# Optimization experiments

Hardware: AMD Instinct MI355X
Metric: run time of the kernel (lower is better)

The kernel has to match this reference:

```python
import jax, jax.numpy as jnp
import numpy as np

EPS = 1e-08


def _phi(x, W):
    # Performer-style positive random features for the softmax kernel.
    # x: [..., d], W: [d, m]
    d = x.shape[-1]
    m = W.shape[-1]
    proj = jnp.einsum('...d,dm->...m', x, W) * (d ** -0.25)
    sq = jnp.sum(x * x, axis=-1, keepdims=True) / (2.0 * jnp.sqrt(jnp.float32(d)))
    return jnp.exp(proj - sq) * (m ** -0.5)


def setup_inputs() -> dict:
    key = jax.random.key(0)
    k1, k2, k3 = jax.random.split(key, 3)
    B, L, D = 8, 2048, 512
    K = 4
    m = 256
    content_amp = jax.random.normal(k1, (B, L, D), dtype=jnp.float32)
    style_amp = jax.random.normal(k2, (B, K, L, D), dtype=jnp.float32)
    W = jax.random.normal(k3, (D, m), dtype=jnp.float32)
    return {"content_amp": content_amp, "style_amp": style_amp, "W": W}


def reference(content_amp, style_amp, W):
    B, K, L, D = style_amp.shape
    style_seq = style_amp.reshape(B, K * L, D)          # [B, KL, D]
    phi_q = _phi(content_amp, W)                         # [B, Lq, m]
    phi_k = _phi(style_seq, W)                           # [B, KL, m]
    S = jnp.einsum('bkm,bkd->bmd', phi_k, style_seq)     # [B, m, D]
    Z = jnp.sum(phi_k, axis=1)                           # [B, m]
    num = jnp.einsum('blm,bmd->bld', phi_q, S)           # [B, Lq, D]
    den = jnp.einsum('blm,bm->bl', phi_q, Z)[..., None] + EPS
    f_a = num / den
    amp_updated = content_amp + f_a
    return (amp_updated, f_a)
```

## Files before the change

### kernel.cpp

```cpp
#include <hip/hip_runtime.h>
#include <hip/hip_bf16.h>
#include <math.h>

typedef short  s16x8 __attribute__((ext_vector_type(8)));
typedef short  s16x4 __attribute__((ext_vector_type(4)));
typedef float  f32x4 __attribute__((ext_vector_type(4)));

#define DD 512
#define MM 256
#define BB 8
#define LL 2048
#define KLT 8192

#define S1f     0.21022410381342864f
#define INV2SDf 0.02209708691207961f
#define S2f     0.0625f
#define EPSV    1e-8f

__device__ __forceinline__ ushort f2b(float f) {
    __hip_bfloat16 h = __float2bfloat16(f);
    return *reinterpret_cast<ushort*>(&h);
}
__device__ __forceinline__ float b2f(ushort u) {
    union { unsigned u32; float f; } x; x.u32 = ((unsigned)u) << 16; return x.f;
}

__global__ __launch_bounds__(256) void convert_rows(const float* __restrict__ X,
                                                    ushort* __restrict__ Xb,
                                                    float* __restrict__ Sq) {
    const int row  = blockIdx.x * 4 + (threadIdx.x >> 6);
    const int lane = threadIdx.x & 63;
    const float4* src = (const float4*)(X + (size_t)row * DD);
    float4 v0 = src[lane];
    float4 v1 = src[lane + 64];
    float s = v0.x * v0.x + v0.y * v0.y + v0.z * v0.z + v0.w * v0.w
            + v1.x * v1.x + v1.y * v1.y + v1.z * v1.z + v1.w * v1.w;
    s16x4* dst = (s16x4*)(Xb + (size_t)row * DD);
    s16x4 o0, o1;
    o0[0] = (short)f2b(v0.x); o0[1] = (short)f2b(v0.y);
    o0[2] = (short)f2b(v0.z); o0[3] = (short)f2b(v0.w);
    o1[0] = (short)f2b(v1.x); o1[1] = (short)f2b(v1.y);
    o1[2] = (short)f2b(v1.z); o1[3] = (short)f2b(v1.w);
    dst[lane]      = o0;
    dst[lane + 64] = o1;
#pragma unroll
    for (int off = 32; off; off >>= 1) s += __shfl_down(s, off);
    if (lane == 0) Sq[row] = s * INV2SDf;
}

__global__ __launch_bounds__(256) void prep_w(const float* __restrict__ W,
                                              ushort* __restrict__ Wt) {
    __shared__ ushort lds[64 * 78];
    const int t = threadIdx.x;
    const int dt = blockIdx.x;
    const int mt = blockIdx.y;
    {
        int r = t >> 2, c0 = (t & 3) * 16;
        const float4* src = (const float4*)(W + (size_t)(dt * 64 + r) * MM + mt * 64 + c0);
#pragma unroll
        for (int i = 0; i < 4; ++i) {
            float4 v = src[i];
            lds[r * 78 + c0 + 4 * i + 0] = f2b(v.x);
            lds[r * 78 + c0 + 4 * i + 1] = f2b(v.y);
            lds[r * 78 + c0 + 4 * i + 2] = f2b(v.z);
            lds[r * 78 + c0 + 4 * i + 3] = f2b(v.w);
        }
    }
    __syncthreads();
    {
        int m = t >> 2, d0 = (t & 3) * 16;
        ushort* dst = Wt + (size_t)(mt * 64 + m) * DD + dt * 64 + d0;
#pragma unroll
        for (int j = 0; j < 16; ++j) dst[j] = lds[(d0 + j) * 78 + m];
    }
}

__global__ __launch_bounds__(256) void transpose_k(const ushort* __restrict__ Sb,
                                                   ushort* __restrict__ StyT) {
    __shared__ ushort lds[64 * 72];
    const int t = threadIdx.x;
    const int klt = blockIdx.x;
    const int dt  = blockIdx.y;
    const int b   = blockIdx.z;
    {
        int r = t >> 2, c0 = (t & 3) * 16;
        const ushort* src = Sb + ((size_t)b * KLT + klt * 64 + r) * DD + dt * 64 + c0;
        *(s16x8*)(lds + r * 72 + c0)     = *(const s16x8*)(src);
        *(s16x8*)(lds + r * 72 + c0 + 8) = *(const s16x8*)(src + 8);
    }
    __syncthreads();
    {
        int d = t >> 2, k0 = (t & 3) * 16;
        s16x8 o0, o1;
#pragma unroll
        for (int j = 0; j < 8; ++j) o0[j] = (short)lds[(k0 + j) * 72 + d];
#pragma unroll
        for (int j = 0; j < 8; ++j) o1[j] = (short)lds[(k0 + 8 + j) * 72 + d];
        ushort* dst = StyT + ((size_t)b * DD + dt * 64 + d) * KLT + klt * 64 + k0;
        *(s16x8*)(dst)     = o0;
        *(s16x8*)(dst + 8) = o1;
    }
}

__device__ __forceinline__ void gemm128(const ushort* __restrict__ A, int lda,
                                        const ushort* __restrict__ B, int ldb,
                                        int rowbase, int colbase, int k0, int k1,
                                        ushort* sA, ushort* sB, f32x4 acc[4][4]) {
    const int t = threadIdx.x;
    const int l = t & 63, w = t >> 6;
    const int wr = (w >> 1) * 64, wc = (w & 1) * 64;
    const int fr = l & 15, fg = l >> 4;
    const int srow = t >> 1, shalf = t & 1;

    for (int kk = k0; kk < k1; kk += 32) {
        {
            const ushort* src = A + (size_t)(rowbase + srow) * lda + kk + shalf * 16;
            *(s16x8*)(sA + srow * 40 + shalf * 16)     = *(const s16x8*)(src);
            *(s16x8*)(sA + srow * 40 + shalf * 16 + 8) = *(const s16x8*)(src + 8);
        }
        {
            const ushort* src = B + (size_t)(colbase + srow) * ldb + kk + shalf * 16;
            *(s16x8*)(sB + srow * 40 + shalf * 16)     = *(const s16x8*)(src);
            *(s16x8*)(sB + srow * 40 + shalf * 16 + 8) = *(const s16x8*)(src + 8);
        }
        __syncthreads();
        s16x8 a[4], b[4];
#pragma unroll
        for (int mi = 0; mi < 4; ++mi)
            a[mi] = *(const s16x8*)(sA + (wr + mi * 16 + fr) * 40 + fg * 8);
#pragma unroll
        for (int ni = 0; ni < 4; ++ni)
            b[ni] = *(const s16x8*)(sB + (wc + ni * 16 + fr) * 40 + fg * 8);
#pragma unroll
        for (int mi = 0; mi < 4; ++mi)
#pragma unroll
            for (int ni = 0; ni < 4; ++ni)
                acc[mi][ni] = __builtin_amdgcn_mfma_f32_16x16x32_bf16(
                    a[mi], b[ni], acc[mi][ni], 0, 0, 0);
        __syncthreads();
    }
}

__global__ __launch_bounds__(256) void phikt_gemm(const ushort* __restrict__ Wt,
                                                  const ushort* __restrict__ Sb,
                                                  const float* __restrict__ sqk,
                                                  ushort* __restrict__ PhiKT) {
    __shared__ __align__(16) ushort sA[128 * 40];
    __shared__ __align__(16) ushort sB[128 * 40];
    f32x4 acc[4][4] = {};
    const int rowbase = blockIdx.y * 128;
    const int colbase = blockIdx.x * 128;
    gemm128(Wt, DD, Sb, DD, rowbase, colbase, 0, DD, sA, sB, acc);

    const int t = threadIdx.x, l = t & 63, w = t >> 6;
    const int wr = (w >> 1) * 64, wc = (w & 1) * 64, fr = l & 15, fg = l >> 4;
    const int b = colbase >> 13;
    const int kll_base = colbase & (KLT - 1);
#pragma unroll
    for (int ni = 0; ni < 4; ++ni) {
        const int klg = colbase + wc + ni * 16 + fr;
        const int kll = kll_base + wc + ni * 16 + fr;
        const float sqv = sqk[klg];
#pragma unroll
        for (int mi = 0; mi < 4; ++mi)
#pragma unroll
            for (int rr = 0; rr < 4; ++rr) {
                const int m = rowbase + wr + mi * 16 + fg * 4 + rr;
                float v = __expf(acc[mi][ni][rr] * S1f - sqv) * S2f;
                PhiKT[((size_t)b << 21) + ((size_t)m << 13) + kll] = f2b(v);
            }
    }
}

__global__ __launch_bounds__(256) void phiq_gemm(const ushort* __restrict__ Cb,
                                                 const ushort* __restrict__ Wt,
                                                 const float* __restrict__ sqq,
                                                 ushort* __restrict__ PhiQ) {
    __shared__ __align__(16) ushort sA[128 * 40];
    __shared__ __align__(16) ushort sB[128 * 40];
    f32x4 acc[4][4] = {};
    const int rowbase = blockIdx.x * 128;
    const int colbase = blockIdx.y * 128;
    gemm128(Cb, DD, Wt, DD, rowbase, colbase, 0, DD, sA, sB, acc);

    const int t = threadIdx.x, l = t & 63, w = t >> 6;
    const int wr = (w >> 1) * 64, wc = (w & 1) * 64, fr = l & 15, fg = l >> 4;
#pragma unroll
    for (int mi = 0; mi < 4; ++mi)
#pragma unroll
        for (int rr = 0; rr < 4; ++rr) {
            const int lg = rowbase + wr + mi * 16 + fg * 4 + rr;
            const float sqv = sqq[lg];
#pragma unroll
            for (int ni = 0; ni < 4; ++ni) {
                const int m = colbase + wc + ni * 16 + fr;
                float v = __expf(acc[mi][ni][rr] * S1f - sqv) * S2f;
                PhiQ[(size_t)lg * MM + m] = f2b(v);
            }
        }
}

__global__ __launch_bounds__(256) void s_gemm(const ushort* __restrict__ PhiKT,
                                              const ushort* __restrict__ StyT,
                                              float* __restrict__ S) {
    __shared__ __align__(16) ushort sA[128 * 40];
    __shared__ __align__(16) ushort sB[128 * 40];
    f32x4 acc[4][4] = {};
    const int b = blockIdx.z >> 3, split = blockIdx.z & 7;
    const int rowbase = blockIdx.x * 128;
    const int colbase = blockIdx.y * 128;
    const ushort* A = PhiKT + ((size_t)b << 21);
    const ushort* B = StyT + (size_t)b * DD * KLT;
    gemm128(A, KLT, B, KLT, rowbase, colbase, split * 1024, split * 1024 + 1024,
            sA, sB, acc);

    const int t = threadIdx.x, l = t & 63, w = t >> 6;
    const int wr = (w >> 1) * 64, wc = (w & 1) * 64, fr = l & 15, fg = l >> 4;
#pragma unroll
    for (int mi = 0; mi < 4; ++mi)
#pragma unroll
        for (int ni = 0; ni < 4; ++ni)
#pragma unroll
            for (int rr = 0; rr < 4; ++rr) {
                const int m = rowbase + wr + mi * 16 + fg * 4 + rr;
                const int d = colbase + wc + ni * 16 + fr;
                atomicAdd(&S[((size_t)b * MM + m) * DD + d], acc[mi][ni][rr]);
            }
}

__global__ __launch_bounds__(256) void s_fin(const float* __restrict__ S,
                                             ushort* __restrict__ St) {
    __shared__ ushort lds[64 * 78];
    const int t = threadIdx.x;
    const int mt = blockIdx.x, dt = blockIdx.y, b = blockIdx.z;
    {
        int r = t >> 2, c0 = (t & 3) * 16;
        const float4* src =
            (const float4*)(S + ((size_t)b * MM + mt * 64 + r) * DD + dt * 64 + c0);
#pragma unroll
        for (int i = 0; i < 4; ++i) {
            float4 v = src[i];
            lds[r * 78 + c0 + 4 * i + 0] = f2b(v.x);
            lds[r * 78 + c0 + 4 * i + 1] = f2b(v.y);
            lds[r * 78 + c0 + 4 * i + 2] = f2b(v.z);
            lds[r * 78 + c0 + 4 * i + 3] = f2b(v.w);
        }
    }
    __syncthreads();
    {
        int d = t >> 2, m0 = (t & 3) * 16;
        ushort* dst = St + ((size_t)b * DD + dt * 64 + d) * MM + mt * 64 + m0;
#pragma unroll
        for (int j = 0; j < 16; ++j) dst[j] = lds[(m0 + j) * 78 + d];
    }
}

__global__ __launch_bounds__(256) void z_kernel(const ushort* __restrict__ PhiKT,
                                                float* __restrict__ Z) {
    const int row = blockIdx.x * 4 + (threadIdx.x >> 6);
    const int lane = threadIdx.x & 63;
    const int b = row >> 8, m = row & 255;
    const ushort* p = PhiKT + ((size_t)b << 21) + ((size_t)m << 13);
    float s = 0.f;
#pragma unroll
    for (int i = 0; i < 16; ++i) {
        s16x8 v = *(const s16x8*)(p + (size_t)(i * 64 + lane) * 8);
#pragma unroll
        for (int j = 0; j < 8; ++j) s += b2f((ushort)v[j]);
    }
#pragma unroll
    for (int off = 32; off; off >>= 1) s += __shfl_down(s, off);
    if (lane == 0) Z[row] = s;
}

__global__ __launch_bounds__(256) void den_kernel(const ushort* __restrict__ PhiQ,
                                                  const float* __restrict__ Z,
                                                  float* __restrict__ Den) {
    const int row = blockIdx.x * 4 + (threadIdx.x >> 6);
    const int lane = threadIdx.x & 63;
    const int b = row >> 11;
    s16x4 q = *(const s16x4*)(PhiQ + (size_t)row * MM + lane * 4);
    float4 z = *(const float4*)(Z + (size_t)b * MM + lane * 4);
    float s = b2f((ushort)q[0]) * z.x + b2f((ushort)q[1]) * z.y +
              b2f((ushort)q[2]) * z.z + b2f((ushort)q[3]) * z.w;
#pragma unroll
    for (int off = 32; off; off >>= 1) s += __shfl_down(s, off);
    if (lane == 0) Den[row] = s;
}

__global__ __launch_bounds__(256) void out_gemm(const ushort* __restrict__ PhiQ,
                                                const ushort* __restrict__ St,
                                                const float* __restrict__ Den,
                                                const float* __restrict__ Content,
                                                float* __restrict__ Amp,
                                                float* __restrict__ Fa) {
    __shared__ __align__(16) ushort sA[128 * 40];
    __shared__ __align__(16) ushort sB[128 * 40];
    f32x4 acc[4][4] = {};
    const int b = blockIdx.z;
    const int rowbase = blockIdx.x * 128;
    const int colbase = blockIdx.y * 128;
    const ushort* A = PhiQ + (size_t)b * LL * MM;
    const ushort* B = St + (size_t)b * DD * MM;
    gemm128(A, MM, B, MM, rowbase, colbase, 0, MM, sA, sB, acc);

    const int t = threadIdx.x, l = t & 63, w = t >> 6;
    const int wr = (w >> 1) * 64, wc = (w & 1) * 64, fr = l & 15, fg = l >> 4;
#pragma unroll
    for (int mi = 0; mi < 4; ++mi)
#pragma unroll
        for (int rr = 0; rr < 4; ++rr) {
            const int lg = b * LL + rowbase + wr + mi * 16 + fg * 4 + rr;
            const float inv = 1.0f / (Den[lg] + EPSV);
#pragma unroll
            for (int ni = 0; ni < 4; ++ni) {
                const int d = colbase + wc + ni * 16 + fr;
                const size_t idx = (size_t)lg * DD + d;
                const float f = acc[mi][ni][rr] * inv;
                Fa[idx] = f;
                Amp[idx] = Content[idx] + f;
            }
        }
}

extern "C" void kernel_launch(void* const* d_in, const int* in_sizes, int n_in,
                              void* d_out, int out_size, void* d_ws, size_t ws_size,
                              hipStream_t stream) {
    const float* content = (const float*)d_in[0];
    const float* style   = (const float*)d_in[1];
    const float* Wm      = (const float*)d_in[2];
    float* amp = (float*)d_out;
    float* fa  = (float*)d_out + (size_t)BB * LL * DD;

    ushort* styleT = (ushort*)d_out;

    float* wsf   = (float*)d_ws;
    float* Sbuf  = wsf;
    float* sq_k  = Sbuf + (size_t)BB * MM * DD;
    float* sq_q  = sq_k + (size_t)BB * KLT;
    float* Zbuf  = sq_q + (size_t)BB * LL;
    float* den   = Zbuf + (size_t)BB * MM;
    ushort* wsu     = (ushort*)(den + (size_t)BB * LL);
    ushort* style_b = wsu;
    ushort* cont_b  = style_b + (size_t)BB * KLT * DD;
    ushort* Wt      = cont_b + (size_t)BB * LL * DD;
    ushort* phi_kT  = Wt + (size_t)MM * DD;
    ushort* phi_q   = phi_kT + (size_t)BB * MM * KLT;
    ushort* St      = phi_q + (size_t)BB * LL * MM;

    hipMemsetAsync(Sbuf, 0, (size_t)BB * MM * DD * sizeof(float), stream);

    prep_w<<<dim3(8, 4), 256, 0, stream>>>(Wm, Wt);
    convert_rows<<<(BB * LL) / 4, 256, 0, stream>>>(content, cont_b, sq_q);
    convert_rows<<<(BB * KLT) / 4, 256, 0, stream>>>(style, style_b, sq_k);

    phikt_gemm<<<dim3((BB * KLT) / 128, MM / 128), 256, 0, stream>>>(Wt, style_b, sq_k, phi_kT);
    phiq_gemm<<<dim3((BB * LL) / 128, MM / 128), 256, 0, stream>>>(cont_b, Wt, sq_q, phi_q);

    transpose_k<<<dim3(KLT / 64, DD / 64, BB), 256, 0, stream>>>(style_b, styleT);

    z_kernel<<<(BB * MM) / 4, 256, 0, stream>>>(phi_kT, Zbuf);
    s_gemm<<<dim3(MM / 128, DD / 128, BB * 8), 256, 0, stream>>>(phi_kT, styleT, Sbuf);
    s_fin<<<dim3(MM / 64, DD / 64, BB), 256, 0, stream>>>(Sbuf, St);

    den_kernel<<<(BB * LL) / 4, 256, 0, stream>>>(phi_q, Zbuf, den);
    out_gemm<<<dim3(LL / 128, DD / 128, BB), 256, 0, stream>>>(phi_q, St, den, content, amp, fa);
}
```

Before: 443.6 us.

## Fuse style conversion with transpose, use direct global-to-LDS loads, drop S atomics

Style bf16 conversion, squared-norm computation and the transpose now run in one kernel, which removes a separate pass over the bf16 style tensor. The shared GEMM loader switches to global_load_lds, writing global memory straight into unpadded LDS tiles. The split-K S GEMM writes per-split partial buffers that s_fin sums, replacing float atomics and their memset. The unpadded LDS layout may add bank conflicts, the partial buffers need more workspace, and row norms are now accumulated with atomics.

```diff
diff --git a/kernel.cpp b/kernel.cpp
--- a/kernel.cpp
+++ b/kernel.cpp
@@ -11,6 +11,7 @@
 #define BB 8
 #define LL 2048
 #define KLT 8192
+#define NSPLIT 8
 
 #define S1f     0.21022410381342864f
 #define INV2SDf 0.02209708691207961f
@@ -23,6 +24,13 @@
 }
 __device__ __forceinline__ float b2f(ushort u) {
     union { unsigned u32; float f; } x; x.u32 = ((unsigned)u) << 16; return x.f;
+}
+
+__device__ __forceinline__ void gl_lds16(const ushort* g, ushort* l) {
+    __builtin_amdgcn_global_load_lds(
+        (const __attribute__((address_space(1))) unsigned int*)(const void*)g,
+        (__attribute__((address_space(3))) unsigned int*)(void*)l,
+        16, 0, 0);
 }
 
 __global__ __launch_bounds__(256) void convert_rows(const float* __restrict__ X,
@@ -48,6 +56,50 @@
     if (lane == 0) Sq[row] = s * INV2SDf;
 }
 
+__global__ __launch_bounds__(256) void conv_style(const float* __restrict__ X,
+                                                  ushort* __restrict__ Xb,
+                                                  ushort* __restrict__ XT,
+                                                  float* __restrict__ Sq) {
+    __shared__ ushort lds[64 * 72];
+    const int t = threadIdx.x;
+    const int klt = blockIdx.x, dt = blockIdx.y, b = blockIdx.z;
+    const int r = t >> 2, c0 = (t & 3) * 16;
+    const size_t rowg = (size_t)b * KLT + klt * 64 + r;
+    const float4* src = (const float4*)(X + rowg * DD + dt * 64 + c0);
+    float s = 0.f;
+    s16x8 o0, o1;
+#pragma unroll
+    for (int i = 0; i < 2; ++i) {
+        float4 v = src[2 * i], w = src[2 * i + 1];
+        s += v.x * v.x + v.y * v.y + v.z * v.z + v.w * v.w
+           + w.x * w.x + w.y * w.y + w.z * w.z + w.w * w.w;
+        s16x8 o;
+        o[0] = (short)f2b(v.x); o[1] = (short)f2b(v.y);
+        o[2] = (short)f2b(v.z); o[3] = (short)f2b(v.w);
+        o[4] = (short)f2b(w.x); o[5] = (short)f2b(w.y);
+        o[6] = (short)f2b(w.z); o[7] = (short)f2b(w.w);
+        if (i == 0) o0 = o; else o1 = o;
+    }
+    ushort* dstb = Xb + rowg * DD + dt * 64 + c0;
+    *(s16x8*)(dstb)     = o0;
+    *(s16x8*)(dstb + 8) = o1;
+    *(s16x8*)(lds + r * 72 + c0)     = o0;
+    *(s16x8*)(lds + r * 72 + c0 + 8) = o1;
+    s += __shfl_xor(s, 1);
+    s += __shfl_xor(s, 2);
+    if ((t & 3) == 0) atomicAdd(&Sq[rowg], s * INV2SDf);
+    __syncthreads();
+    const int d = t >> 2, k0c = (t & 3) * 16;
+    s16x8 t0, t1;
+#pragma unroll
+    for (int j = 0; j < 8; ++j) t0[j] = (short)lds[(k0c + j) * 72 + d];
+#pragma unroll
+    for (int j = 0; j < 8; ++j) t1[j] = (short)lds[(k0c + 8 + j) * 72 + d];
+    ushort* dstT = XT + ((size_t)b * DD + dt * 64 + d) * KLT + klt * 64 + k0c;
+    *(s16x8*)(dstT)     = t0;
+    *(s16x8*)(dstT + 8) = t1;
+}
+
 __global__ __launch_bounds__(256) void prep_w(const float* __restrict__ W,
                                               ushort* __restrict__ Wt) {
     __shared__ ushort lds[64 * 78];
@@ -75,33 +127,6 @@
     }
 }
 
-__global__ __launch_bounds__(256) void transpose_k(const ushort* __restrict__ Sb,
-                                                   ushort* __restrict__ StyT) {
-    __shared__ ushort lds[64 * 72];
-    const int t = threadIdx.x;
-    const int klt = blockIdx.x;
-    const int dt  = blockIdx.y;
-    const int b   = blockIdx.z;
-    {
-        int r = t >> 2, c0 = (t & 3) * 16;
-        const ushort* src = Sb + ((size_t)b * KLT + klt * 64 + r) * DD + dt * 64 + c0;
-        *(s16x8*)(lds + r * 72 + c0)     = *(const s16x8*)(src);
-        *(s16x8*)(lds + r * 72 + c0 + 8) = *(const s16x8*)(src + 8);
-    }
-    __syncthreads();
-    {
-        int d = t >> 2, k0 = (t & 3) * 16;
-        s16x8 o0, o1;
-#pragma unroll
-        for (int j = 0; j < 8; ++j) o0[j] = (short)lds[(k0 + j) * 72 + d];
-#pragma unroll
-        for (int j = 0; j < 8; ++j) o1[j] = (short)lds[(k0 + 8 + j) * 72 + d];
-        ushort* dst = StyT + ((size_t)b * DD + dt * 64 + d) * KLT + klt * 64 + k0;
-        *(s16x8*)(dst)     = o0;
-        *(s16x8*)(dst + 8) = o1;
-    }
-}
-
 __device__ __forceinline__ void gemm128(const ushort* __restrict__ A, int lda,
                                         const ushort* __restrict__ B, int ldb,
                                         int rowbase, int colbase, int k0, int k1,
@@ -110,27 +135,25 @@
     const int l = t & 63, w = t >> 6;
     const int wr = (w >> 1) * 64, wc = (w & 1) * 64;
     const int fr = l & 15, fg = l >> 4;
-    const int srow = t >> 1, shalf = t & 1;
+    const int lrow = l >> 2, lk = (l & 3) * 8;
 
     for (int kk = k0; kk < k1; kk += 32) {
-        {
-            const ushort* src = A + (size_t)(rowbase + srow) * lda + kk + shalf * 16;
-            *(s16x8*)(sA + srow * 40 + shalf * 16)     = *(const s16x8*)(src);
-            *(s16x8*)(sA + srow * 40 + shalf * 16 + 8) = *(const s16x8*)(src + 8);
-        }
-        {
-            const ushort* src = B + (size_t)(colbase + srow) * ldb + kk + shalf * 16;
-            *(s16x8*)(sB + srow * 40 + shalf * 16)     = *(const s16x8*)(src);
-            *(s16x8*)(sB + srow * 40 + shalf * 16 + 8) = *(const s16x8*)(src + 8);
-        }
+        gl_lds16(A + (size_t)(rowbase + w * 16 + lrow) * lda + kk + lk,
+                 sA + (w * 16) * 32);
+        gl_lds16(A + (size_t)(rowbase + (w + 4) * 16 + lrow) * lda + kk + lk,
+                 sA + ((w + 4) * 16) * 32);
+        gl_lds16(B + (size_t)(colbase + w * 16 + lrow) * ldb + kk + lk,
+                 sB + (w * 16) * 32);
+        gl_lds16(B + (size_t)(colbase + (w + 4) * 16 + lrow) * ldb + kk + lk,
+                 sB + ((w + 4) * 16) * 32);
         __syncthreads();
         s16x8 a[4], b[4];
 #pragma unroll
         for (int mi = 0; mi < 4; ++mi)
-            a[mi] = *(const s16x8*)(sA + (wr + mi * 16 + fr) * 40 + fg * 8);
+            a[mi] = *(const s16x8*)(sA + (wr + mi * 16 + fr) * 32 + fg * 8);
 #pragma unroll
         for (int ni = 0; ni < 4; ++ni)
-            b[ni] = *(const s16x8*)(sB + (wc + ni * 16 + fr) * 40 + fg * 8);
+            b[ni] = *(const s16x8*)(sB + (wc + ni * 16 + fr) * 32 + fg * 8);
 #pragma unroll
         for (int mi = 0; mi < 4; ++mi)
 #pragma unroll
@@ -145,8 +168,8 @@
                                                   const ushort* __restrict__ Sb,
                                                   const float* __restrict__ sqk,
                                                   ushort* __restrict__ PhiKT) {
-    __shared__ __align__(16) ushort sA[128 * 40];
-    __shared__ __align__(16) ushort sB[128 * 40];
+    __shared__ __align__(16) ushort sA[128 * 32];
+    __shared__ __align__(16) ushort sB[128 * 32];
     f32x4 acc[4][4] = {};
     const int rowbase = blockIdx.y * 128;
     const int colbase = blockIdx.x * 128;
@@ -176,8 +199,8 @@
                                                  const ushort* __restrict__ Wt,
                                                  const float* __restrict__ sqq,
                                                  ushort* __restrict__ PhiQ) {
-    __shared__ __align__(16) ushort sA[128 * 40];
-    __shared__ __align__(16) ushort sB[128 * 40];
+    __shared__ __align__(16) ushort sA[128 * 32];
+    __shared__ __align__(16) ushort sB[128 * 32];
     f32x4 acc[4][4] = {};
     const int rowbase = blockIdx.x * 128;
     const int colbase = blockIdx.y * 128;
@@ -202,9 +225,9 @@
 
 __global__ __launch_bounds__(256) void s_gemm(const ushort* __restrict__ PhiKT,
                                               const ushort* __restrict__ StyT,
-                                              float* __restrict__ S) {
-    __shared__ __align__(16) ushort sA[128 * 40];
-    __shared__ __align__(16) ushort sB[128 * 40];
+                                              float* __restrict__ Spart) {
+    __shared__ __align__(16) ushort sA[128 * 32];
+    __shared__ __align__(16) ushort sB[128 * 32];
     f32x4 acc[4][4] = {};
     const int b = blockIdx.z >> 3, split = blockIdx.z & 7;
     const int rowbase = blockIdx.x * 128;
@@ -216,6 +239,7 @@
 
     const int t = threadIdx.x, l = t & 63, w = t >> 6;
     const int wr = (w >> 1) * 64, wc = (w & 1) * 64, fr = l & 15, fg = l >> 4;
+    float* out = Spart + (size_t)(split * BB + b) * MM * DD;
 #pragma unroll
     for (int mi = 0; mi < 4; ++mi)
 #pragma unroll
@@ -224,31 +248,37 @@
             for (int rr = 0; rr < 4; ++rr) {
                 const int m = rowbase + wr + mi * 16 + fg * 4 + rr;
                 const int d = colbase + wc + ni * 16 + fr;
-                atomicAdd(&S[((size_t)b * MM + m) * DD + d], acc[mi][ni][rr]);
-            }
-}
-
-__global__ __launch_bounds__(256) void s_fin(const float* __restrict__ S,
+                out[(size_t)m * DD + d] = acc[mi][ni][rr];
+            }
+}
+
+__global__ __launch_bounds__(256) void s_fin(const float* __restrict__ Sp,
                                              ushort* __restrict__ St) {
     __shared__ ushort lds[64 * 78];
     const int t = threadIdx.x;
     const int mt = blockIdx.x, dt = blockIdx.y, b = blockIdx.z;
     {
-        int r = t >> 2, c0 = (t & 3) * 16;
-        const float4* src =
-            (const float4*)(S + ((size_t)b * MM + mt * 64 + r) * DD + dt * 64 + c0);
-#pragma unroll
-        for (int i = 0; i < 4; ++i) {
-            float4 v = src[i];
-            lds[r * 78 + c0 + 4 * i + 0] = f2b(v.x);
-            lds[r * 78 + c0 + 4 * i + 1] = f2b(v.y);
-            lds[r * 78 + c0 + 4 * i + 2] = f2b(v.z);
-            lds[r * 78 + c0 + 4 * i + 3] = f2b(v.w);
+        const int r = t >> 2, c0 = (t & 3) * 16;
+        float accv[16];
+#pragma unroll
+        for (int j = 0; j < 16; ++j) accv[j] = 0.f;
+#pragma unroll
+        for (int sp = 0; sp < NSPLIT; ++sp) {
+            const float4* src = (const float4*)(Sp +
+                ((size_t)(sp * BB + b) * MM + mt * 64 + r) * DD + dt * 64 + c0);
+#pragma unroll
+            for (int i = 0; i < 4; ++i) {
+                float4 v = src[i];
+                accv[4 * i + 0] += v.x; accv[4 * i + 1] += v.y;
+                accv[4 * i + 2] += v.z; accv[4 * i + 3] += v.w;
+            }
         }
+#pragma unroll
+        for (int j = 0; j < 16; ++j) lds[r * 78 + c0 + j] = f2b(accv[j]);
     }
     __syncthreads();
     {
-        int d = t >> 2, m0 = (t & 3) * 16;
+        const int d = t >> 2, m0 = (t & 3) * 16;
         ushort* dst = St + ((size_t)b * DD + dt * 64 + d) * MM + mt * 64 + m0;
 #pragma unroll
         for (int j = 0; j < 16; ++j) dst[j] = lds[(m0 + j) * 78 + d];
@@ -294,8 +324,8 @@
                                                 const float* __restrict__ Content,
                                                 float* __restrict__ Amp,
                                                 float* __restrict__ Fa) {
-    __shared__ __align__(16) ushort sA[128 * 40];
-    __shared__ __align__(16) ushort sB[128 * 40];
+    __shared__ __align__(16) ushort sA[128 * 32];
+    __shared__ __align__(16) ushort sB[128 * 32];
     f32x4 acc[4][4] = {};
     const int b = blockIdx.z;
     const int rowbase = blockIdx.x * 128;
@@ -335,8 +365,8 @@
     ushort* styleT = (ushort*)d_out;
 
     float* wsf   = (float*)d_ws;
-    float* Sbuf  = wsf;
-    float* sq_k  = Sbuf + (size_t)BB * MM * DD;
+    float* Spart = wsf;
+    float* sq_k  = Spart + (size_t)NSPLIT * BB * MM * DD;
     float* sq_q  = sq_k + (size_t)BB * KLT;
     float* Zbuf  = sq_q + (size_t)BB * LL;
     float* den   = Zbuf + (size_t)BB * MM;
@@ -348,20 +378,18 @@
     ushort* phi_q   = phi_kT + (size_t)BB * MM * KLT;
     ushort* St      = phi_q + (size_t)BB * LL * MM;
 
-    hipMemsetAsync(Sbuf, 0, (size_t)BB * MM * DD * sizeof(float), stream);
+    hipMemsetAsync(sq_k, 0, (size_t)BB * KLT * sizeof(float), stream);
 
     prep_w<<<dim3(8, 4), 256, 0, stream>>>(Wm, Wt);
     convert_rows<<<(BB * LL) / 4, 256, 0, stream>>>(content, cont_b, sq_q);
-    convert_rows<<<(BB * KLT) / 4, 256, 0, stream>>>(style, style_b, sq_k);
+    conv_style<<<dim3(KLT / 64, DD / 64, BB), 256, 0, stream>>>(style, style_b, styleT, sq_k);
 
     phikt_gemm<<<dim3((BB * KLT) / 128, MM / 128), 256, 0, stream>>>(Wt, style_b, sq_k, phi_kT);
     phiq_gemm<<<dim3((BB * LL) / 128, MM / 128), 256, 0, stream>>>(cont_b, Wt, sq_q, phi_q);
 
-    transpose_k<<<dim3(KLT / 64, DD / 64, BB), 256, 0, stream>>>(style_b, styleT);
-
     z_kernel<<<(BB * MM) / 4, 256, 0, stream>>>(phi_kT, Zbuf);
-    s_gemm<<<dim3(MM / 128, DD / 128, BB * 8), 256, 0, stream>>>(phi_kT, styleT, Sbuf);
-    s_fin<<<dim3(MM / 64, DD / 64, BB), 256, 0, stream>>>(Sbuf, St);
+    s_gemm<<<dim3(MM / 128, DD / 128, BB * NSPLIT), 256, 0, stream>>>(phi_kT, styleT, Spart);
+    s_fin<<<dim3(MM / 64, DD / 64, BB), 256, 0, stream>>>(Spart, St);
 
     den_kernel<<<(BB * LL) / 4, 256, 0, stream>>>(phi_q, Zbuf, den);
     out_gemm<<<dim3(LL / 128, DD / 128, BB), 256, 0, stream>>>(phi_q, St, den, content, amp, fa);
```

New measurement: 419.0 us. -5.5%, faster.
